# Kernel optimization log

Measured on AMD Instinct MI355X. Metric: run time of the kernel, lower is better.

The kernel has to match this reference:

```python
import jax, jax.numpy as jnp
import numpy as np

B, N, C = 2, 2048, 512
HEADS, WINDOW, R = 8, 64, 8
LORA_SCALE = 2.0 / R  # alpha / r


def setup_inputs() -> dict:
    key = jax.random.key(0)
    ks = jax.random.split(key, 8)
    def w(k, shp, sc=0.02):
        return (jax.random.normal(k, shp, jnp.float32) * sc)
    return {
        "x": jax.random.normal(ks[0], (B, N, C), jnp.float32),
        "w_qkv": w(ks[1], (C, 3 * C)),              # qkv Linear (bias=False), stored [in,out]
        "lora_A_qkv": w(ks[2], (C, R), 0.01),
        "lora_B_qkv": w(ks[3], (R, 3 * C), 0.01),
        "w_out": w(ks[4], (C, C)),                  # out Linear, stored [in,out]
        "b_out": jnp.zeros((C,), jnp.float32),
        "lora_A_out": w(ks[5], (C, R), 0.01),
        "lora_B_out": w(ks[6], (R, C), 0.01),
    }


def reference(x, w_qkv, lora_A_qkv, lora_B_qkv, w_out, b_out, lora_A_out, lora_B_out):
    b, n, c = x.shape
    dh = c // HEADS
    scale = dh ** -0.5

    # qkv projection with LoRA (LoRALayer: base(x) + x@A@B * alpha/r)
    qkv = x @ w_qkv + (x @ lora_A_qkv) @ lora_B_qkv * LORA_SCALE
    qkv = qkv.reshape(b, n, 3, HEADS, dh)
    q = jnp.transpose(qkv[:, :, 0], (0, 2, 1, 3))  # [b,h,n,dh]
    k = jnp.transpose(qkv[:, :, 1], (0, 2, 1, 3))
    v = jnp.transpose(qkv[:, :, 2], (0, 2, 1, 3))

    # local branch: dense scores, causal AND band |i-j| <= WINDOW
    scores = jnp.einsum('bhid,bhjd->bhij', q, k) * scale
    i = jnp.arange(n)[:, None]
    j = jnp.arange(n)[None, :]
    valid = (j <= i) & (jnp.abs(i - j) <= WINDOW)  # causal & local band
    scores = jnp.where(valid[None, None], scores, -jnp.inf)
    attn = jax.nn.softmax(scores, axis=-1)
    out_local = jnp.einsum('bhij,bhjd->bhid', attn, v)

    # global branch: strided keys/values every WINDOW steps; causal_g is all-ones
    # in the source, so no masking -> plain softmax over strided keys.
    kg = k[:, :, ::WINDOW, :]
    vg = v[:, :, ::WINDOW, :]
    sg = jnp.einsum('bhid,bhjd->bhij', q, kg) * scale
    ag = jax.nn.softmax(sg, axis=-1)
    out_global = jnp.einsum('bhij,bhjd->bhid', ag, vg)

    out = (out_local + out_global).transpose(0, 2, 1, 3).reshape(b, n, c)
    # output projection with LoRA
    return out @ w_out + b_out + (out @ lora_A_out) @ lora_B_out * LORA_SCALE
```

## Files before the change

kernel.cpp:

```cpp
#include <hip/hip_runtime.h>

#define N_SEQ 2048
#define CDIM 512
#define HEADS 8
#define DH 64
#define WINDOW 64
#define BATCH 2
#define KP 544

typedef __attribute__((ext_vector_type(8))) short bf16x8;
typedef __attribute__((ext_vector_type(4))) short short4v;
typedef __attribute__((ext_vector_type(8))) short short8v;
typedef __attribute__((ext_vector_type(4))) float f32x4;

__device__ __forceinline__ unsigned short f2b(float f){
  unsigned u = __float_as_uint(f);
  unsigned r = (u + 0x7fffu + ((u >> 16) & 1u)) >> 16;
  return (unsigned short)r;
}
__device__ __forceinline__ float b2f(unsigned short h){ return __uint_as_float(((unsigned)h) << 16); }

__device__ __forceinline__ void gl_lds16(const void* g, void* l){
  __builtin_amdgcn_global_load_lds(
      (const __attribute__((address_space(1))) void*)g,
      (__attribute__((address_space(3))) void*)l, 16, 0, 0);
}

__global__ __launch_bounds__(256) void prep(
    const float* __restrict__ x, const float* __restrict__ lA_qkv,
    const float* __restrict__ w_qkv, const float* __restrict__ lB_qkv,
    const float* __restrict__ w_out, const float* __restrict__ lB_out,
    const float* __restrict__ lA_out,
    short* __restrict__ A1, short* __restrict__ wT1,
    short* __restrict__ wT2, short* __restrict__ lBo, short* __restrict__ lAT){
  __shared__ float T[64][65];
  const int bx = blockIdx.x, tid = threadIdx.x;
  if (bx < 1024){
    const int w = tid >> 6, lane = tid & 63;
    const int m = bx*4 + w;
    const float4* row = (const float4*)(x + (size_t)m*CDIM);
    float acc[8] = {0.f,0.f,0.f,0.f,0.f,0.f,0.f,0.f};
    #pragma unroll
    for (int hh = 0; hh < 2; hh++){
      float4 v = row[hh*64 + lane];
      int c = hh*256 + lane*4;
      short4v pk;
      pk[0] = (short)f2b(v.x); pk[1] = (short)f2b(v.y);
      pk[2] = (short)f2b(v.z); pk[3] = (short)f2b(v.w);
      *(short4v*)&A1[(size_t)m*KP + c] = pk;
      float e[4] = {v.x, v.y, v.z, v.w};
      #pragma unroll
      for (int q = 0; q < 4; q++){
        const float* ar = lA_qkv + (size_t)(c + q)*8;
        #pragma unroll
        for (int r = 0; r < 8; r++) acc[r] += e[q]*ar[r];
      }
    }
    #pragma unroll
    for (int r = 0; r < 8; r++){
      #pragma unroll
      for (int off = 32; off; off >>= 1) acc[r] += __shfl_xor(acc[r], off);
    }
    float myv = 0.f;
    #pragma unroll
    for (int r = 0; r < 8; r++) if (lane == r) myv = acc[r];
    if (lane < 32) A1[(size_t)m*KP + 512 + lane] = (lane < 8) ? (short)f2b(myv) : (short)0;
    return;
  }
  if (bx < 1216 || (bx >= 1240 && bx < 1304)){
    const float* wsrc; short* dst; int NN, STR, ct, kt;
    if (bx < 1216){ int bxx = bx - 1024; wsrc = w_qkv; dst = wT1; NN = 1536; STR = KP;  ct = bxx % 24; kt = bxx / 24; }
    else          { int bxx = bx - 1240; wsrc = w_out; dst = wT2; NN = 512;  STR = 512; ct = bxx % 8;  kt = bxx / 8; }
    const int n0 = ct*64, k0 = kt*64;
    #pragma unroll
    for (int it = 0; it < 16; it++){
      int r = (tid >> 6) + it*4, c = tid & 63;
      T[r][c] = wsrc[(size_t)(k0 + r)*NN + n0 + c];
    }
    __syncthreads();
    #pragma unroll
    for (int it = 0; it < 16; it++){
      int rw = (tid >> 6) + it*4, cw = tid & 63;
      dst[(size_t)(n0 + rw)*STR + k0 + cw] = (short)f2b(T[cw][rw]);
    }
    return;
  }
  if (bx < 1240){
    const int n = (bx - 1216)*64 + (tid & 63);
    const int quarter = tid >> 6;
    short8v pk;
    #pragma unroll
    for (int i = 0; i < 8; i++){
      int j = quarter*8 + i;
      pk[i] = (j < 8) ? (short)f2b(0.25f * lB_qkv[(size_t)j*1536 + n]) : (short)0;
    }
    *(short8v*)&wT1[(size_t)n*KP + 512 + quarter*8] = pk;
    return;
  }
  if (bx < 1306){
    int n = (bx - 1304)*256 + tid;
    short8v pk;
    #pragma unroll
    for (int r = 0; r < 8; r++) pk[r] = (short)f2b(0.25f * lB_out[(size_t)r*512 + n]);
    *(short8v*)&lBo[(size_t)n*8] = pk;
    return;
  }
  for (int t = tid; t < 16*512; t += 256){
    int r = t >> 9, k = t & 511;
    lAT[t] = (r < 8) ? (short)f2b(lA_out[(size_t)k*8 + r]) : (short)0;
  }
}

__global__ __launch_bounds__(256) void gemm_qkv(const short* __restrict__ A,
    const short* __restrict__ Bt,
    short* __restrict__ qb, short* __restrict__ kb,
    short* __restrict__ vT, short* __restrict__ vgT){
  __shared__ __align__(16) short SMEM[24576];
  short* AsB = SMEM;
  short* BsB = SMEM + 12288;
  const int tid = threadIdx.x;
  const int wid = tid >> 6, lane = tid & 63;
  const int ln = lane & 15, lg = lane >> 4;
  const int phys = blockIdx.y*12 + blockIdx.x;
  const int s = (phys & 7)*48 + (phys >> 3);
  const int m0 = (s/12)*128, n0 = (s%12)*128;
  const int wr = wid >> 1, wc = wid & 1;
  f32x4 acc[4][4];
  #pragma unroll
  for (int mi = 0; mi < 4; mi++)
    #pragma unroll
    for (int ni = 0; ni < 4; ni++){ f32x4 z = {0.f,0.f,0.f,0.f}; acc[mi][ni] = z; }

  auto stage = [&](int k0, int buf){
    #pragma unroll
    for (int i = 0; i < 2; i++){
      int li = i*256 + tid;
      int row = li >> 2, p = li & 3;
      int sl = p ^ ((row >> 1) & 3);
      gl_lds16(&A[(size_t)(m0 + row)*KP + k0 + sl*8], &AsB[buf*4096 + (i*256 + wid*64)*8]);
    }
    #pragma unroll
    for (int i = 0; i < 2; i++){
      int li = i*256 + tid;
      int row = li >> 2, p = li & 3;
      int sl = p ^ ((row >> 1) & 3);
      gl_lds16(&Bt[(size_t)(n0 + row)*KP + k0 + sl*8], &BsB[buf*4096 + (i*256 + wid*64)*8]);
    }
  };
  auto compute = [&](int buf){
    bf16x8 af[4], bfr[4];
    #pragma unroll
    for (int mi = 0; mi < 4; mi++){
      int row = wr*64 + mi*16 + ln;
      af[mi] = *(const bf16x8*)&AsB[buf*4096 + row*32 + ((lg ^ ((row >> 1) & 3)) << 3)];
    }
    #pragma unroll
    for (int ni = 0; ni < 4; ni++){
      int row = wc*64 + ni*16 + ln;
      bfr[ni] = *(const bf16x8*)&BsB[buf*4096 + row*32 + ((lg ^ ((row >> 1) & 3)) << 3)];
    }
    #pragma unroll
    for (int mi = 0; mi < 4; mi++)
      #pragma unroll
      for (int ni = 0; ni < 4; ni++)
        acc[mi][ni] = __builtin_amdgcn_mfma_f32_16x16x32_bf16(af[mi], bfr[ni], acc[mi][ni], 0, 0, 0);
  };

  stage(0, 0);
  stage(32, 1);
  for (int kt = 0; kt < 17; kt++){
    if (kt < 16) asm volatile("s_waitcnt vmcnt(4)" ::: "memory");
    else         asm volatile("s_waitcnt vmcnt(0)" ::: "memory");
    __builtin_amdgcn_s_barrier();
    __builtin_amdgcn_sched_barrier(0);
    if (kt < 15) stage((kt+2)*32, (kt+2)%3);
    compute(kt%3);
    asm volatile("s_waitcnt lgkmcnt(0)" ::: "memory");
    __builtin_amdgcn_sched_barrier(0);
    __builtin_amdgcn_s_barrier();
  }

  short* Ct = SMEM;
  #pragma unroll
  for (int mi = 0; mi < 4; mi++){
    int mrow = wr*64 + mi*16 + lg*4;
    #pragma unroll
    for (int ni = 0; ni < 4; ni++){
      int ncol = wc*64 + ni*16 + ln;
      #pragma unroll
      for (int r = 0; r < 4; r++)
        Ct[(mrow + r)*136 + ncol] = (short)f2b(acc[mi][ni][r]);
    }
  }
  __syncthreads();
  const int sq = n0 >> 9;
  const int b = m0 >> 11, nseqb = m0 & 2047;
  const int h0 = (n0 & 511) >> 6;
  if (sq < 2){
    short* dstbase = (sq == 0 ? qb : kb);
    #pragma unroll
    for (int c = 0; c < 8; c++){
      int m = c*16 + (tid >> 4);
      int n = (tid & 15) * 8;
      bf16x8 v = *(const bf16x8*)&Ct[m*136 + n];
      int bh = b*8 + h0 + (n >> 6);
      *(bf16x8*)&dstbase[(size_t)bh*131072 + (size_t)(nseqb + m)*64 + (n & 63)] = v;
    }
  } else {
    const int w2 = tid >> 7;
    const int n = tid & 127;
    const int bh = b*8 + h0 + (n >> 6);
    const int d = n & 63;
    #pragma unroll
    for (int c = 0; c < 8; c++){
      int mb = w2*64 + c*8;
      short tmp0, tmp1, tmp2, tmp3, tmp4, tmp5, tmp6, tmp7;
      tmp0 = Ct[(mb+0)*136 + n]; tmp1 = Ct[(mb+1)*136 + n];
      tmp2 = Ct[(mb+2)*136 + n]; tmp3 = Ct[(mb+3)*136 + n];
      tmp4 = Ct[(mb+4)*136 + n]; tmp5 = Ct[(mb+5)*136 + n];
      tmp6 = Ct[(mb+6)*136 + n]; tmp7 = Ct[(mb+7)*136 + n];
      bf16x8 v = {tmp0, tmp1, tmp2, tmp3, tmp4, tmp5, tmp6, tmp7};
      *(bf16x8*)&vT[(size_t)bh*131072 + (size_t)d*2048 + (nseqb + mb)] = v;
    }
    {
      int gl = tid >> 7, nn = tid & 127;
      int mrel = gl*64;
      int bh2 = b*8 + h0 + (nn >> 6);
      int d2 = nn & 63;
      vgT[(size_t)bh2*2048 + d2*32 + ((nseqb + mrel) >> 6)] = Ct[mrel*136 + nn];
    }
  }
}

__global__ __launch_bounds__(256) void attn_mfma(const short* __restrict__ qb,
    const short* __restrict__ kb, const short* __restrict__ vT,
    const short* __restrict__ vgT, short* __restrict__ A2){
  __shared__ __align__(16) short Ps[4][16][168];
  const int phys = blockIdx.y*32 + blockIdx.x;
  const int s = (phys & 7)*64 + (phys >> 3);
  const int qt = s & 31, bh = s >> 5;
  const int qbase = qt * 64;
  const int tid = threadIdx.x, w = tid >> 6, lane = tid & 63;
  const int ln = lane & 15, lg = lane >> 4;
  const size_t base = (size_t)bh * (N_SEQ * DH);
  const short* Qp = qb + base;
  const short* Kp = kb + base;
  const short* Vt = vT + base;
  const short* Vg = vgT + (size_t)bh * (DH * 32);
  const int i = qbase + w*16 + ln;
  const int kwin0 = qbase - 64;

  bf16x8 qf[2];
  #pragma unroll
  for (int ks = 0; ks < 2; ks++)
    qf[ks] = *(const bf16x8*)&Qp[(size_t)i*DH + ks*32 + lg*8];

  f32x4 sL[8], sG[2];
  #pragma unroll
  for (int f = 0; f < 8; f++){ f32x4 z = {0.f,0.f,0.f,0.f}; sL[f] = z; }
  #pragma unroll
  for (int f = 0; f < 2; f++){ f32x4 z = {0.f,0.f,0.f,0.f}; sG[f] = z; }
  #pragma unroll
  for (int f = 0; f < 8; f++){
    const short* kr = Kp + (long long)(kwin0 + f*16 + ln) * DH;
    #pragma unroll
    for (int ks = 0; ks < 2; ks++){
      bf16x8 kf = *(const bf16x8*)&kr[ks*32 + lg*8];
      sL[f] = __builtin_amdgcn_mfma_f32_16x16x32_bf16(kf, qf[ks], sL[f], 0, 0, 0);
    }
  }
  #pragma unroll
  for (int fg = 0; fg < 2; fg++){
    const short* kr = Kp + (size_t)(fg*16 + ln) * (WINDOW * DH);
    #pragma unroll
    for (int ks = 0; ks < 2; ks++){
      bf16x8 kf = *(const bf16x8*)&kr[ks*32 + lg*8];
      sG[fg] = __builtin_amdgcn_mfma_f32_16x16x32_bf16(kf, qf[ks], sG[fg], 0, 0, 0);
    }
  }

  float mx = -1e30f;
  #pragma unroll
  for (int f = 0; f < 8; f++){
    #pragma unroll
    for (int r = 0; r < 4; r++){
      int j = kwin0 + 16*f + lg*4 + r;
      bool valid = (j >= 0) && (j <= i) && (i - j <= WINDOW);
      float sv = valid ? sL[f][r] * 0.125f : -1e30f;
      sL[f][r] = sv;
      mx = fmaxf(mx, sv);
    }
  }
  mx = fmaxf(mx, __shfl_xor(mx, 16));
  mx = fmaxf(mx, __shfl_xor(mx, 32));
  float sum = 0.f;
  #pragma unroll
  for (int f = 0; f < 8; f++){
    #pragma unroll
    for (int r = 0; r < 4; r++){
      float p = __expf(sL[f][r] - mx);
      sL[f][r] = p;
      sum += p;
    }
  }
  sum += __shfl_xor(sum, 16);
  sum += __shfl_xor(sum, 32);
  float inv = 1.f / sum;
  #pragma unroll
  for (int f = 0; f < 8; f++){
    short4v pk;
    #pragma unroll
    for (int r = 0; r < 4; r++) pk[r] = (short)f2b(sL[f][r] * inv);
    *(short4v*)&Ps[w][ln][16*f + 4*lg] = pk;
  }
  float mg = -1e30f;
  #pragma unroll
  for (int fg = 0; fg < 2; fg++)
    #pragma unroll
    for (int r = 0; r < 4; r++){
      float sv = sG[fg][r] * 0.125f;
      sG[fg][r] = sv;
      mg = fmaxf(mg, sv);
    }
  mg = fmaxf(mg, __shfl_xor(mg, 16));
  mg = fmaxf(mg, __shfl_xor(mg, 32));
  float sg2 = 0.f;
  #pragma unroll
  for (int fg = 0; fg < 2; fg++)
    #pragma unroll
    for (int r = 0; r < 4; r++){
      float p = __expf(sG[fg][r] - mg);
      sG[fg][r] = p;
      sg2 += p;
    }
  sg2 += __shfl_xor(sg2, 16);
  sg2 += __shfl_xor(sg2, 32);
  float invg = 1.f / sg2;
  #pragma unroll
  for (int fg = 0; fg < 2; fg++){
    short4v pk;
    #pragma unroll
    for (int r = 0; r < 4; r++) pk[r] = (short)f2b(sG[fg][r] * invg);
    *(short4v*)&Ps[w][ln][128 + 16*fg + 4*lg] = pk;
  }
  __syncthreads();

  bf16x8 pa[5];
  #pragma unroll
  for (int ks = 0; ks < 5; ks++)
    pa[ks] = *(const bf16x8*)&Ps[w][ln][ks*32 + lg*8];
  f32x4 o[4];
  #pragma unroll
  for (int n16 = 0; n16 < 4; n16++){ f32x4 z = {0.f,0.f,0.f,0.f}; o[n16] = z; }
  #pragma unroll
  for (int n16 = 0; n16 < 4; n16++){
    int d = n16*16 + ln;
    #pragma unroll
    for (int ks = 0; ks < 4; ks++){
      bf16x8 vv = *(const bf16x8*)&Vt[(long long)d*N_SEQ + kwin0 + ks*32 + lg*8];
      o[n16] = __builtin_amdgcn_mfma_f32_16x16x32_bf16(pa[ks], vv, o[n16], 0, 0, 0);
    }
    bf16x8 vv = *(const bf16x8*)&Vg[d*32 + lg*8];
    o[n16] = __builtin_amdgcn_mfma_f32_16x16x32_bf16(pa[4], vv, o[n16], 0, 0, 0);
  }

  const int h = bh & 7, b = bh >> 3;
  #pragma unroll
  for (int n16 = 0; n16 < 4; n16++){
    int d = n16*16 + ln;
    #pragma unroll
    for (int r = 0; r < 4; r++){
      int qrow = qbase + 16*w + lg*4 + r;
      A2[(size_t)(b*N_SEQ + qrow)*CDIM + h*DH + d] = (short)f2b(o[n16][r]);
    }
  }
}

__global__ __launch_bounds__(256) void gemm_out(const short* __restrict__ A,
    const short* __restrict__ Bt, const short* __restrict__ lBo,
    const short* __restrict__ lAT, const float* __restrict__ bias,
    float* __restrict__ outp){
  __shared__ __align__(16) short As[64*32];
  __shared__ __align__(16) short Bs[128*32];
  __shared__ float aoLDS[64][8];
  const int tid = threadIdx.x;
  const int wid = tid >> 6, lane = tid & 63;
  const int ln = lane & 15, lg = lane >> 4;
  const int phys = blockIdx.y*4 + blockIdx.x;
  const int s = (phys & 7)*32 + (phys >> 3);
  const int m0 = (s >> 2)*64, n0 = (s & 3)*128;
  const int wr = wid >> 1, wc = wid & 1;
  f32x4 acc[2][4];
  f32x4 aoacc[2];
  #pragma unroll
  for (int mi = 0; mi < 2; mi++){
    f32x4 z = {0.f,0.f,0.f,0.f};
    aoacc[mi] = z;
    #pragma unroll
    for (int ni = 0; ni < 4; ni++) acc[mi][ni] = z;
  }

  for (int kt = 0; kt < 16; kt++){
    const int k0 = kt*32;
    if (kt) __syncthreads();
    {
      int row = tid >> 2, p = tid & 3;
      int sl = p ^ ((row >> 1) & 3);
      gl_lds16(&A[(size_t)(m0 + row)*CDIM + k0 + sl*8], &As[(wid*64)*8]);
    }
    #pragma unroll
    for (int i = 0; i < 2; i++){
      int li = i*256 + tid;
      int row = li >> 2, p = li & 3;
      int sl = p ^ ((row >> 1) & 3);
      gl_lds16(&Bt[(size_t)(n0 + row)*CDIM + k0 + sl*8], &Bs[(i*256 + wid*64)*8]);
    }
    asm volatile("s_waitcnt vmcnt(0)" ::: "memory");
    __syncthreads();
    bf16x8 af[2], bfr[4];
    #pragma unroll
    for (int mi = 0; mi < 2; mi++){
      int row = wr*32 + mi*16 + ln;
      af[mi] = *(const bf16x8*)&As[row*32 + ((lg ^ ((row >> 1) & 3)) << 3)];
    }
    #pragma unroll
    for (int ni = 0; ni < 4; ni++){
      int row = wc*64 + ni*16 + ln;
      bfr[ni] = *(const bf16x8*)&Bs[row*32 + ((lg ^ ((row >> 1) & 3)) << 3)];
    }
    bf16x8 bfl = *(const bf16x8*)&lAT[(size_t)ln*512 + k0 + lg*8];
    #pragma unroll
    for (int mi = 0; mi < 2; mi++){
      aoacc[mi] = __builtin_amdgcn_mfma_f32_16x16x32_bf16(af[mi], bfl, aoacc[mi], 0, 0, 0);
      #pragma unroll
      for (int ni = 0; ni < 4; ni++)
        acc[mi][ni] = __builtin_amdgcn_mfma_f32_16x16x32_bf16(af[mi], bfr[ni], acc[mi][ni], 0, 0, 0);
    }
  }

  if (wc == 0 && ln < 8){
    #pragma unroll
    for (int mi = 0; mi < 2; mi++)
      #pragma unroll
      for (int j = 0; j < 4; j++)
        aoLDS[wr*32 + mi*16 + lg*4 + j][ln] = aoacc[mi][j];
  }
  __syncthreads();

  #pragma unroll
  for (int mi = 0; mi < 2; mi++){
    #pragma unroll
    for (int j = 0; j < 4; j++){
      int rl = wr*32 + mi*16 + lg*4 + j;
      int m = m0 + rl;
      float ao8[8];
      #pragma unroll
      for (int r = 0; r < 8; r++) ao8[r] = aoLDS[rl][r];
      #pragma unroll
      for (int ni = 0; ni < 4; ni++){
        int jg = n0 + wc*64 + ni*16 + ln;
        bf16x8 lbv = *(const bf16x8*)&lBo[(size_t)jg*8];
        float lora = 0.f;
        #pragma unroll
        for (int r = 0; r < 8; r++) lora += ao8[r] * b2f((unsigned short)lbv[r]);
        outp[(size_t)m*CDIM + jg] = acc[mi][ni][j] + bias[jg] + lora;
      }
    }
  }
}

extern "C" void kernel_launch(void* const* d_in, const int* in_sizes, int n_in,
                              void* d_out, int out_size, void* d_ws, size_t ws_size,
                              hipStream_t stream){
  const float* x      = (const float*)d_in[0];
  const float* w_qkv  = (const float*)d_in[1];
  const float* lA_qkv = (const float*)d_in[2];
  const float* lB_qkv = (const float*)d_in[3];
  const float* w_out  = (const float*)d_in[4];
  const float* b_out  = (const float*)d_in[5];
  const float* lA_out = (const float*)d_in[6];
  const float* lB_out = (const float*)d_in[7];
  float* out = (float*)d_out;

  short* A1  = (short*)d_ws;
  short* wT1 = A1  + (size_t)4096*KP;
  short* wT2 = wT1 + (size_t)1536*KP;
  short* lBo = wT2 + (size_t)512*512;
  short* lAT = lBo + (size_t)512*8;
  short* qb  = lAT + (size_t)16*512;
  short* kb  = qb  + (size_t)16*2048*64;
  short* vT  = kb  + (size_t)16*2048*64;
  short* vgT = vT  + (size_t)16*2048*64;
  short* A2  = vgT + (size_t)16*64*32;

  prep<<<1307, 256, 0, stream>>>(x, lA_qkv, w_qkv, lB_qkv, w_out, lB_out, lA_out,
                                 A1, wT1, wT2, lBo, lAT);
  gemm_qkv<<<dim3(12, 32), 256, 0, stream>>>(A1, wT1, qb, kb, vT, vgT);
  attn_mfma<<<dim3(32, 16), 256, 0, stream>>>(qb, kb, vT, vgT, A2);
  gemm_out<<<dim3(4, 64), 256, 0, stream>>>(A2, wT2, lBo, lAT, b_out, out);
}
```

Measured before the change: 61.10 us.

## Fold LoRA adapters into base weights and pipeline output GEMM

The prep kernel now merges each LoRA pair into its dense weight, computing W + scale*A@B while transposing to bf16. This removes the extra K=32 LoRA slice from the QKV GEMM (K drops from 544 to 512) and the separate LoRA MFMA and epilogue in the output GEMM. The output GEMM also gains the same triple-buffered global-to-LDS pipeline already used by the QKV GEMM. The trade-off is that the merged low-rank term is now rounded to bf16 together with the base weight.

```diff
diff --git a/kernel.cpp b/kernel.cpp
--- a/kernel.cpp
+++ b/kernel.cpp
@@ -6,11 +6,9 @@
 #define DH 64
 #define WINDOW 64
 #define BATCH 2
-#define KP 544
 
 typedef __attribute__((ext_vector_type(8))) short bf16x8;
 typedef __attribute__((ext_vector_type(4))) short short4v;
-typedef __attribute__((ext_vector_type(8))) short short8v;
 typedef __attribute__((ext_vector_type(4))) float f32x4;
 
 __device__ __forceinline__ unsigned short f2b(float f){
@@ -27,87 +25,50 @@
 }
 
 __global__ __launch_bounds__(256) void prep(
-    const float* __restrict__ x, const float* __restrict__ lA_qkv,
-    const float* __restrict__ w_qkv, const float* __restrict__ lB_qkv,
-    const float* __restrict__ w_out, const float* __restrict__ lB_out,
-    const float* __restrict__ lA_out,
-    short* __restrict__ A1, short* __restrict__ wT1,
-    short* __restrict__ wT2, short* __restrict__ lBo, short* __restrict__ lAT){
-  __shared__ float T[64][65];
+    const float* __restrict__ x,
+    const float* __restrict__ w_qkv, const float* __restrict__ lA_qkv, const float* __restrict__ lB_qkv,
+    const float* __restrict__ w_out, const float* __restrict__ lA_out, const float* __restrict__ lB_out,
+    short* __restrict__ A1, short* __restrict__ wT1, short* __restrict__ wT2){
   const int bx = blockIdx.x, tid = threadIdx.x;
-  if (bx < 1024){
-    const int w = tid >> 6, lane = tid & 63;
-    const int m = bx*4 + w;
-    const float4* row = (const float4*)(x + (size_t)m*CDIM);
-    float acc[8] = {0.f,0.f,0.f,0.f,0.f,0.f,0.f,0.f};
-    #pragma unroll
-    for (int hh = 0; hh < 2; hh++){
-      float4 v = row[hh*64 + lane];
-      int c = hh*256 + lane*4;
+  if (bx < 512){
+    #pragma unroll
+    for (int j = 0; j < 4; j++){
+      int g = bx*1024 + j*256 + tid;
+      float4 v = ((const float4*)x)[g];
       short4v pk;
       pk[0] = (short)f2b(v.x); pk[1] = (short)f2b(v.y);
       pk[2] = (short)f2b(v.z); pk[3] = (short)f2b(v.w);
-      *(short4v*)&A1[(size_t)m*KP + c] = pk;
-      float e[4] = {v.x, v.y, v.z, v.w};
-      #pragma unroll
-      for (int q = 0; q < 4; q++){
-        const float* ar = lA_qkv + (size_t)(c + q)*8;
-        #pragma unroll
-        for (int r = 0; r < 8; r++) acc[r] += e[q]*ar[r];
-      }
-    }
-    #pragma unroll
-    for (int r = 0; r < 8; r++){
-      #pragma unroll
-      for (int off = 32; off; off >>= 1) acc[r] += __shfl_xor(acc[r], off);
-    }
-    float myv = 0.f;
-    #pragma unroll
-    for (int r = 0; r < 8; r++) if (lane == r) myv = acc[r];
-    if (lane < 32) A1[(size_t)m*KP + 512 + lane] = (lane < 8) ? (short)f2b(myv) : (short)0;
+      ((short4v*)A1)[g] = pk;
+    }
     return;
   }
-  if (bx < 1216 || (bx >= 1240 && bx < 1304)){
-    const float* wsrc; short* dst; int NN, STR, ct, kt;
-    if (bx < 1216){ int bxx = bx - 1024; wsrc = w_qkv; dst = wT1; NN = 1536; STR = KP;  ct = bxx % 24; kt = bxx / 24; }
-    else          { int bxx = bx - 1240; wsrc = w_out; dst = wT2; NN = 512;  STR = 512; ct = bxx % 8;  kt = bxx / 8; }
-    const int n0 = ct*64, k0 = kt*64;
-    #pragma unroll
-    for (int it = 0; it < 16; it++){
-      int r = (tid >> 6) + it*4, c = tid & 63;
-      T[r][c] = wsrc[(size_t)(k0 + r)*NN + n0 + c];
-    }
-    __syncthreads();
-    #pragma unroll
-    for (int it = 0; it < 16; it++){
-      int rw = (tid >> 6) + it*4, cw = tid & 63;
-      dst[(size_t)(n0 + rw)*STR + k0 + cw] = (short)f2b(T[cw][rw]);
-    }
-    return;
-  }
-  if (bx < 1240){
-    const int n = (bx - 1216)*64 + (tid & 63);
-    const int quarter = tid >> 6;
-    short8v pk;
-    #pragma unroll
-    for (int i = 0; i < 8; i++){
-      int j = quarter*8 + i;
-      pk[i] = (j < 8) ? (short)f2b(0.25f * lB_qkv[(size_t)j*1536 + n]) : (short)0;
-    }
-    *(short8v*)&wT1[(size_t)n*KP + 512 + quarter*8] = pk;
-    return;
-  }
-  if (bx < 1306){
-    int n = (bx - 1304)*256 + tid;
-    short8v pk;
-    #pragma unroll
-    for (int r = 0; r < 8; r++) pk[r] = (short)f2b(0.25f * lB_out[(size_t)r*512 + n]);
-    *(short8v*)&lBo[(size_t)n*8] = pk;
-    return;
-  }
-  for (int t = tid; t < 16*512; t += 256){
-    int r = t >> 9, k = t & 511;
-    lAT[t] = (r < 8) ? (short)f2b(lA_out[(size_t)k*8 + r]) : (short)0;
+  __shared__ float T[64][65];
+  __shared__ float lAs[64][9];
+  __shared__ float lBs[8][64];
+  const float *wsrc, *lA, *lB; short* dst; int NN, ct, kt;
+  if (bx < 704){ int bxx = bx - 512; wsrc = w_qkv; lA = lA_qkv; lB = lB_qkv; dst = wT1; NN = 1536; ct = bxx % 24; kt = bxx / 24; }
+  else         { int bxx = bx - 704; wsrc = w_out; lA = lA_out; lB = lB_out; dst = wT2; NN = 512;  ct = bxx % 8;  kt = bxx / 8; }
+  const int n0 = ct*64, k0 = kt*64;
+  {
+    int t0 = tid, t1 = tid + 256;
+    lAs[t0 >> 3][t0 & 7] = lA[(size_t)(k0 + (t0 >> 3))*8 + (t0 & 7)];
+    lAs[t1 >> 3][t1 & 7] = lA[(size_t)(k0 + (t1 >> 3))*8 + (t1 & 7)];
+    lBs[t0 >> 6][t0 & 63] = lB[(size_t)(t0 >> 6)*NN + n0 + (t0 & 63)];
+    lBs[4 + (t0 >> 6)][t0 & 63] = lB[(size_t)(4 + (t0 >> 6))*NN + n0 + (t0 & 63)];
+  }
+  #pragma unroll
+  for (int it = 0; it < 16; it++){
+    int r = (tid >> 6) + it*4, c = tid & 63;
+    T[r][c] = wsrc[(size_t)(k0 + r)*NN + n0 + c];
+  }
+  __syncthreads();
+  #pragma unroll
+  for (int it = 0; it < 16; it++){
+    int rw = (tid >> 6) + it*4, cw = tid & 63;
+    float lora = 0.f;
+    #pragma unroll
+    for (int r = 0; r < 8; r++) lora += lAs[cw][r] * lBs[r][rw];
+    dst[(size_t)(n0 + rw)*512 + k0 + cw] = (short)f2b(T[cw][rw] + 0.25f*lora);
   }
 }
 
@@ -137,14 +98,14 @@
       int li = i*256 + tid;
       int row = li >> 2, p = li & 3;
       int sl = p ^ ((row >> 1) & 3);
-      gl_lds16(&A[(size_t)(m0 + row)*KP + k0 + sl*8], &AsB[buf*4096 + (i*256 + wid*64)*8]);
+      gl_lds16(&A[(size_t)(m0 + row)*512 + k0 + sl*8], &AsB[buf*4096 + (i*256 + wid*64)*8]);
     }
     #pragma unroll
     for (int i = 0; i < 2; i++){
       int li = i*256 + tid;
       int row = li >> 2, p = li & 3;
       int sl = p ^ ((row >> 1) & 3);
-      gl_lds16(&Bt[(size_t)(n0 + row)*KP + k0 + sl*8], &BsB[buf*4096 + (i*256 + wid*64)*8]);
+      gl_lds16(&Bt[(size_t)(n0 + row)*512 + k0 + sl*8], &BsB[buf*4096 + (i*256 + wid*64)*8]);
     }
   };
   auto compute = [&](int buf){
@@ -168,12 +129,13 @@
 
   stage(0, 0);
   stage(32, 1);
-  for (int kt = 0; kt < 17; kt++){
-    if (kt < 16) asm volatile("s_waitcnt vmcnt(4)" ::: "memory");
+  #pragma unroll 1
+  for (int kt = 0; kt < 16; kt++){
+    if (kt < 15) asm volatile("s_waitcnt vmcnt(4)" ::: "memory");
     else         asm volatile("s_waitcnt vmcnt(0)" ::: "memory");
     __builtin_amdgcn_s_barrier();
     __builtin_amdgcn_sched_barrier(0);
-    if (kt < 15) stage((kt+2)*32, (kt+2)%3);
+    if (kt < 14) stage((kt+2)*32, (kt+2)%3);
     compute(kt%3);
     asm volatile("s_waitcnt lgkmcnt(0)" ::: "memory");
     __builtin_amdgcn_sched_barrier(0);
@@ -214,11 +176,10 @@
     #pragma unroll
     for (int c = 0; c < 8; c++){
       int mb = w2*64 + c*8;
-      short tmp0, tmp1, tmp2, tmp3, tmp4, tmp5, tmp6, tmp7;
-      tmp0 = Ct[(mb+0)*136 + n]; tmp1 = Ct[(mb+1)*136 + n];
-      tmp2 = Ct[(mb+2)*136 + n]; tmp3 = Ct[(mb+3)*136 + n];
-      tmp4 = Ct[(mb+4)*136 + n]; tmp5 = Ct[(mb+5)*136 + n];
-      tmp6 = Ct[(mb+6)*136 + n]; tmp7 = Ct[(mb+7)*136 + n];
+      short tmp0 = Ct[(mb+0)*136 + n], tmp1 = Ct[(mb+1)*136 + n];
+      short tmp2 = Ct[(mb+2)*136 + n], tmp3 = Ct[(mb+3)*136 + n];
+      short tmp4 = Ct[(mb+4)*136 + n], tmp5 = Ct[(mb+5)*136 + n];
+      short tmp6 = Ct[(mb+6)*136 + n], tmp7 = Ct[(mb+7)*136 + n];
       bf16x8 v = {tmp0, tmp1, tmp2, tmp3, tmp4, tmp5, tmp6, tmp7};
       *(bf16x8*)&vT[(size_t)bh*131072 + (size_t)d*2048 + (nseqb + mb)] = v;
     }
@@ -377,12 +338,10 @@
 }
 
 __global__ __launch_bounds__(256) void gemm_out(const short* __restrict__ A,
-    const short* __restrict__ Bt, const short* __restrict__ lBo,
-    const short* __restrict__ lAT, const float* __restrict__ bias,
+    const short* __restrict__ Bt, const float* __restrict__ bias,
     float* __restrict__ outp){
-  __shared__ __align__(16) short As[64*32];
-  __shared__ __align__(16) short Bs[128*32];
-  __shared__ float aoLDS[64][8];
+  __shared__ __align__(16) short AsB[3*2048];
+  __shared__ __align__(16) short BsB[3*4096];
   const int tid = threadIdx.x;
   const int wid = tid >> 6, lane = tid & 63;
   const int ln = lane & 15, lg = lane >> 4;
@@ -391,80 +350,69 @@
   const int m0 = (s >> 2)*64, n0 = (s & 3)*128;
   const int wr = wid >> 1, wc = wid & 1;
   f32x4 acc[2][4];
-  f32x4 aoacc[2];
-  #pragma unroll
-  for (int mi = 0; mi < 2; mi++){
-    f32x4 z = {0.f,0.f,0.f,0.f};
-    aoacc[mi] = z;
-    #pragma unroll
-    for (int ni = 0; ni < 4; ni++) acc[mi][ni] = z;
-  }
-
-  for (int kt = 0; kt < 16; kt++){
-    const int k0 = kt*32;
-    if (kt) __syncthreads();
+  #pragma unroll
+  for (int mi = 0; mi < 2; mi++)
+    #pragma unroll
+    for (int ni = 0; ni < 4; ni++){ f32x4 z = {0.f,0.f,0.f,0.f}; acc[mi][ni] = z; }
+
+  auto stage = [&](int k0, int buf){
     {
       int row = tid >> 2, p = tid & 3;
       int sl = p ^ ((row >> 1) & 3);
-      gl_lds16(&A[(size_t)(m0 + row)*CDIM + k0 + sl*8], &As[(wid*64)*8]);
+      gl_lds16(&A[(size_t)(m0 + row)*CDIM + k0 + sl*8], &AsB[buf*2048 + (wid*64)*8]);
     }
     #pragma unroll
     for (int i = 0; i < 2; i++){
       int li = i*256 + tid;
       int row = li >> 2, p = li & 3;
       int sl = p ^ ((row >> 1) & 3);
-      gl_lds16(&Bt[(size_t)(n0 + row)*CDIM + k0 + sl*8], &Bs[(i*256 + wid*64)*8]);
-    }
-    asm volatile("s_waitcnt vmcnt(0)" ::: "memory");
-    __syncthreads();
+      gl_lds16(&Bt[(size_t)(n0 + row)*CDIM + k0 + sl*8], &BsB[buf*4096 + (i*256 + wid*64)*8]);
+    }
+  };
+  auto compute = [&](int buf){
     bf16x8 af[2], bfr[4];
     #pragma unroll
     for (int mi = 0; mi < 2; mi++){
       int row = wr*32 + mi*16 + ln;
-      af[mi] = *(const bf16x8*)&As[row*32 + ((lg ^ ((row >> 1) & 3)) << 3)];
+      af[mi] = *(const bf16x8*)&AsB[buf*2048 + row*32 + ((lg ^ ((row >> 1) & 3)) << 3)];
     }
     #pragma unroll
     for (int ni = 0; ni < 4; ni++){
       int row = wc*64 + ni*16 + ln;
-      bfr[ni] = *(const bf16x8*)&Bs[row*32 + ((lg ^ ((row >> 1) & 3)) << 3)];
-    }
-    bf16x8 bfl = *(const bf16x8*)&lAT[(size_t)ln*512 + k0 + lg*8];
-    #pragma unroll
-    for (int mi = 0; mi < 2; mi++){
-      aoacc[mi] = __builtin_amdgcn_mfma_f32_16x16x32_bf16(af[mi], bfl, aoacc[mi], 0, 0, 0);
+      bfr[ni] = *(const bf16x8*)&BsB[buf*4096 + row*32 + ((lg ^ ((row >> 1) & 3)) << 3)];
+    }
+    #pragma unroll
+    for (int mi = 0; mi < 2; mi++)
       #pragma unroll
       for (int ni = 0; ni < 4; ni++)
         acc[mi][ni] = __builtin_amdgcn_mfma_f32_16x16x32_bf16(af[mi], bfr[ni], acc[mi][ni], 0, 0, 0);
-    }
-  }
-
-  if (wc == 0 && ln < 8){
-    #pragma unroll
-    for (int mi = 0; mi < 2; mi++)
+  };
+
+  stage(0, 0);
+  stage(32, 1);
+  #pragma unroll 1
+  for (int kt = 0; kt < 16; kt++){
+    if (kt < 15) asm volatile("s_waitcnt vmcnt(3)" ::: "memory");
+    else         asm volatile("s_waitcnt vmcnt(0)" ::: "memory");
+    __builtin_amdgcn_s_barrier();
+    __builtin_amdgcn_sched_barrier(0);
+    if (kt < 14) stage((kt+2)*32, (kt+2)%3);
+    compute(kt%3);
+    asm volatile("s_waitcnt lgkmcnt(0)" ::: "memory");
+    __builtin_amdgcn_sched_barrier(0);
+    __builtin_amdgcn_s_barrier();
+  }
+
+  #pragma unroll
+  for (int mi = 0; mi < 2; mi++){
+    int mbase = m0 + wr*32 + mi*16 + lg*4;
+    #pragma unroll
+    for (int ni = 0; ni < 4; ni++){
+      int jg = n0 + wc*64 + ni*16 + ln;
+      float bi = bias[jg];
       #pragma unroll
-      for (int j = 0; j < 4; j++)
-        aoLDS[wr*32 + mi*16 + lg*4 + j][ln] = aoacc[mi][j];
-  }
-  __syncthreads();
-
-  #pragma unroll
-  for (int mi = 0; mi < 2; mi++){
-    #pragma unroll
-    for (int j = 0; j < 4; j++){
-      int rl = wr*32 + mi*16 + lg*4 + j;
-      int m = m0 + rl;
-      float ao8[8];
-      #pragma unroll
-      for (int r = 0; r < 8; r++) ao8[r] = aoLDS[rl][r];
-      #pragma unroll
-      for (int ni = 0; ni < 4; ni++){
-        int jg = n0 + wc*64 + ni*16 + ln;
-        bf16x8 lbv = *(const bf16x8*)&lBo[(size_t)jg*8];
-        float lora = 0.f;
-        #pragma unroll
-        for (int r = 0; r < 8; r++) lora += ao8[r] * b2f((unsigned short)lbv[r]);
-        outp[(size_t)m*CDIM + jg] = acc[mi][ni][j] + bias[jg] + lora;
-      }
+      for (int r = 0; r < 4; r++)
+        outp[(size_t)(mbase + r)*CDIM + jg] = acc[mi][ni][r] + bi;
     }
   }
 }
@@ -483,19 +431,17 @@
   float* out = (float*)d_out;
 
   short* A1  = (short*)d_ws;
-  short* wT1 = A1  + (size_t)4096*KP;
-  short* wT2 = wT1 + (size_t)1536*KP;
-  short* lBo = wT2 + (size_t)512*512;
-  short* lAT = lBo + (size_t)512*8;
-  short* qb  = lAT + (size_t)16*512;
+  short* wT1 = A1  + (size_t)4096*512;
+  short* wT2 = wT1 + (size_t)1536*512;
+  short* qb  = wT2 + (size_t)512*512;
   short* kb  = qb  + (size_t)16*2048*64;
   short* vT  = kb  + (size_t)16*2048*64;
   short* vgT = vT  + (size_t)16*2048*64;
   short* A2  = vgT + (size_t)16*64*32;
 
-  prep<<<1307, 256, 0, stream>>>(x, lA_qkv, w_qkv, lB_qkv, w_out, lB_out, lA_out,
-                                 A1, wT1, wT2, lBo, lAT);
+  prep<<<768, 256, 0, stream>>>(x, w_qkv, lA_qkv, lB_qkv, w_out, lA_out, lB_out,
+                                A1, wT1, wT2);
   gemm_qkv<<<dim3(12, 32), 256, 0, stream>>>(A1, wT1, qb, kb, vT, vgT);
   attn_mfma<<<dim3(32, 16), 256, 0, stream>>>(qb, kb, vT, vgT, A2);
-  gemm_out<<<dim3(4, 64), 256, 0, stream>>>(A2, wT2, lBo, lAT, b_out, out);
-}
+  gemm_out<<<dim3(4, 64), 256, 0, stream>>>(A2, wT2, b_out, out);
+}
```

Result: faster. 50.12 us (-18.0%).
